# Performance work log

Hardware: AMD Instinct MI355X
Metric: run time of the kernel (lower is better)

The kernel has to match this reference:

```python
import jax, jax.numpy as jnp
import numpy as np

B, S, D, NH = 4, 2048, 1024, 16
HD = D // NH


def setup_inputs() -> dict:
    key = jax.random.key(0)
    ks = jax.random.split(key, 8)
    inp = {
        'value': jax.random.normal(ks[0], (B, S, D), jnp.float32),
        'key_t': jax.random.normal(ks[1], (B, S, D), jnp.float32),
        'query': jax.random.normal(ks[2], (B, S, D), jnp.float32),
        'mask': jnp.ones((B, 1, 1, S), jnp.int32),
        # nn.Linear weights (stored as [out, in]; y = x @ W.T). bias=False for q/k/v.
        'W_q': jax.random.normal(ks[3], (D, D), jnp.float32) * (D ** -0.5),
        'W_k': jax.random.normal(ks[4], (D, D), jnp.float32) * (D ** -0.5),
        'W_v': jax.random.normal(ks[5], (D, D), jnp.float32) * (D ** -0.5),
        'W_o': jax.random.normal(ks[6], (D, D), jnp.float32) * (D ** -0.5),
        'b_o': jax.random.normal(ks[7], (D,), jnp.float32) * 0.01,
    }
    return inp


def _split_head(x):
    b, s, d = x.shape
    return x.reshape(b, s, NH, d // NH).transpose(0, 2, 1, 3)  # [B,NH,S,HD]


def reference(value, key_t, query, mask, W_q, W_k, W_v, W_o, b_o):
    # Linear projections (y = x @ W.T), then split heads
    q = _split_head(query @ W_q.T)  # [B,NH,S,HD]
    k = _split_head(key_t @ W_k.T)
    v = _split_head(value @ W_v.T)

    q = q * (HD ** -0.5)
    att = jnp.einsum('bhqd,bhkd->bhqk', q, k)  # [B,NH,S,S]
    att = jnp.where(mask == 0, -jnp.inf, att)
    att = jax.nn.softmax(att, axis=-1)
    # dropout_ratio = 0.0 -> identity (eval mode)
    ctx = jnp.einsum('bhqk,bhkd->bhqd', att, v)  # [B,NH,S,HD]

    ctx = ctx.transpose(0, 2, 1, 3).reshape(B, S, D)  # concat heads
    out = ctx @ W_o.T + b_o
    out = jax.nn.gelu(out, approximate=False)  # nn.GELU default = exact erf
    return out
```

## Files before the change

### kernel.cpp

```cpp
#include <hip/hip_runtime.h>
#include <hip/hip_bf16.h>

typedef __bf16 bf16;
typedef __bf16 bf16x8 __attribute__((ext_vector_type(8)));
typedef __bf16 bf16x4 __attribute__((ext_vector_type(4)));
typedef float f32x4 __attribute__((ext_vector_type(4)));
typedef float f32x16 __attribute__((ext_vector_type(16)));
typedef unsigned int uint;

#define NB 4
#define NS 2048
#define ND 1024
#define NHH 16
#define NHD 64

__device__ __forceinline__ void gload_lds16(const void* g, void* l) {
  __builtin_amdgcn_global_load_lds((const __attribute__((address_space(1))) void*)g,
                                   (__attribute__((address_space(3))) void*)l, 16, 0, 0);
}

__device__ __forceinline__ f32x4 mfma16(bf16x8 a, bf16x8 b, f32x4 c) {
  return __builtin_amdgcn_mfma_f32_16x16x32_bf16(a, b, c, 0, 0, 0);
}
__device__ __forceinline__ f32x16 mfma32(bf16x8 a, bf16x8 b, f32x16 c) {
  return __builtin_amdgcn_mfma_f32_32x32x16_bf16(a, b, c, 0, 0, 0);
}
__device__ __forceinline__ uint cvtpk(float lo, float hi) {
  uint r;
  asm("v_cvt_pk_bf16_f32 %0, %1, %2" : "=v"(r) : "v"(lo), "v"(hi));
  return r;
}
__device__ __forceinline__ void swap32u(uint& a, uint& b) {
  asm("v_permlane32_swap_b32 %0, %1" : "+v"(a), "+v"(b));
}
__device__ __forceinline__ float expv(float x) {
  float r;
  asm("v_exp_f32 %0, %1" : "=v"(r) : "v"(x));
  return r;
}
#define BARRIER()                          \
  do {                                     \
    asm volatile("" ::: "memory");         \
    __builtin_amdgcn_s_barrier();          \
    asm volatile("" ::: "memory");         \
  } while (0)

__global__ __launch_bounds__(256) void cvt_bf16(const float4* __restrict__ in,
                                                bf16x4* __restrict__ out,
                                                float scale, int n4) {
  int i = blockIdx.x * 256 + threadIdx.x;
  if (i < n4) {
    float4 v = in[i];
    bf16x4 o;
    o[0] = (bf16)(v.x * scale);
    o[1] = (bf16)(v.y * scale);
    o[2] = (bf16)(v.z * scale);
    o[3] = (bf16)(v.w * scale);
    out[i] = o;
  }
}

__global__ __launch_bounds__(256) void prep(
    const float4* __restrict__ w0, const float4* __restrict__ w1,
    const float4* __restrict__ w2, const float4* __restrict__ w3,
    bf16x4* __restrict__ wout, float scale0, int n4each,
    const int* __restrict__ m, float* __restrict__ mb,
    uint* __restrict__ cleanw, int nmask) {
  const int bid = blockIdx.x;
  if (bid < 4096) {
    int i = bid * 256 + threadIdx.x;
    int w = i / n4each;
    int j = i - w * n4each;
    const float4* src = (w == 0) ? w0 : (w == 1) ? w1 : (w == 2) ? w2 : w3;
    float sc = (w == 0) ? scale0 : 1.0f;
    float4 v = src[j];
    bf16x4 o;
    o[0] = (bf16)(v.x * sc);
    o[1] = (bf16)(v.y * sc);
    o[2] = (bf16)(v.z * sc);
    o[3] = (bf16)(v.w * sc);
    wout[i] = o;
  } else if (bid < 4128) {
    int i = (bid - 4096) * 256 + threadIdx.x;
    if (i < nmask) mb[i] = m[i] ? 0.0f : -3e38f;
  } else {
    int i = threadIdx.x;
    if (i < 128) {
      const int* p = m + i * 64;
      int all1 = 1;
#pragma unroll
      for (int j = 0; j < 64; j += 4) {
        int4 v = *(const int4*)(p + j);
        all1 &= (v.x && v.y && v.z && v.w) ? 1 : 0;
      }
      unsigned long long bal = __ballot(all1);
      int wv = i >> 6, lane = i & 63;
      if (lane == 0) {
        cleanw[2 * wv] = (uint)bal;
        cleanw[2 * wv + 1] = (uint)(bal >> 32);
      }
    }
  }
}

template <int EPI>
__global__ __launch_bounds__(256) void gemm8(
    const bf16* __restrict__ A, const bf16* __restrict__ Bw,
    bf16* __restrict__ Cb, float* __restrict__ Cf,
    const float* __restrict__ bias, int M, int N, int K) {
  __shared__ bf16 As[3][4096];
  __shared__ bf16 Bs[3][4096];
  bf16* As0 = &As[0][0];
  bf16* Bs0 = &Bs[0][0];
  const int tid = threadIdx.x;
  const int lane = tid & 63, wv = tid >> 6;
  const int wr = wv >> 1, wc = wv & 1;
  const int g = lane >> 4, r = lane & 15;
  const int nx = N >> 7;
  const int chunk = gridDim.x >> 3;
  const int bid = blockIdx.x;
  const int wg = (bid & 7) * chunk + (bid >> 3);
  const int colBase = (wg % nx) * 128;
  const int rowBase = (wg / nx) * 128;

  const int sRow = wv * 16 + (lane >> 2);
  const int sK = ((lane & 3) ^ ((lane >> 3) & 3)) * 8;
  const bf16* aj0 = A + (long)(rowBase + sRow) * K + sK;
  const bf16* aj1 = aj0 + 64L * K;
  const bf16* bj0 = Bw + (long)(colBase + sRow) * K + sK;
  const bf16* bj1 = bj0 + 64L * K;

#define GSTAGE(bi, kk)                                      \
  do {                                                      \
    gload_lds16(aj0 + (kk), As0 + (bi) * 4096 + wv * 512);  \
    gload_lds16(aj1 + (kk), As0 + (bi) * 4096 + 2048 + wv * 512); \
    gload_lds16(bj0 + (kk), Bs0 + (bi) * 4096 + wv * 512);  \
    gload_lds16(bj1 + (kk), Bs0 + (bi) * 4096 + 2048 + wv * 512); \
  } while (0)

  f32x4 acc[4][4] = {};
  const int gs = (g ^ ((r >> 1) & 3)) * 8;

  GSTAGE(0, 0);
  GSTAGE(1, 32);
  int cur = 0, nxt2 = 2;

  for (int k0 = 0; k0 < K; k0 += 32) {
    if (k0 + 32 < K) {
      asm volatile("s_waitcnt vmcnt(4)" ::: "memory");
    } else {
      asm volatile("s_waitcnt vmcnt(0)" ::: "memory");
    }
    BARRIER();
    __builtin_amdgcn_sched_barrier(0);
    if (k0 + 64 < K) GSTAGE(nxt2, k0 + 64);

    const bf16* Ac = As0 + cur * 4096;
    const bf16* Bc = Bs0 + cur * 4096;
    bf16x8 af[4], bfr[4];
#pragma unroll
    for (int m = 0; m < 4; m++)
      af[m] = *(const bf16x8*)(Ac + (wr * 64 + m * 16 + r) * 32 + gs);
#pragma unroll
    for (int n = 0; n < 4; n++)
      bfr[n] = *(const bf16x8*)(Bc + (wc * 64 + n * 16 + r) * 32 + gs);
    __builtin_amdgcn_s_setprio(1);
#pragma unroll
    for (int m = 0; m < 4; m++)
#pragma unroll
      for (int n = 0; n < 4; n++)
        acc[m][n] = mfma16(af[m], bfr[n], acc[m][n]);
    __builtin_amdgcn_s_setprio(0);
    cur = (cur == 2) ? 0 : cur + 1;
    nxt2 = (nxt2 == 2) ? 0 : nxt2 + 1;
  }
#undef GSTAGE

  if (EPI == 0) {
#pragma unroll
    for (int m = 0; m < 4; m++)
#pragma unroll
      for (int n = 0; n < 4; n++)
#pragma unroll
        for (int q = 0; q < 4; q++) {
          int row = rowBase + wr * 64 + m * 16 + 4 * g + q;
          int col = colBase + wc * 64 + n * 16 + r;
          Cb[(long)row * N + col] = (bf16)acc[m][n][q];
        }
  } else if (EPI == 1) {
    const int b = rowBase >> 11;
    const int sbase = (rowBase & 2047) + wr * 64;
#pragma unroll
    for (int m = 0; m < 4; m++) {
#pragma unroll
      for (int n = 0; n < 4; n++) {
        int col = colBase + wc * 64 + n * 16 + r;
        int h = col >> 6, d = col & 63;
        bf16x4 pk;
#pragma unroll
        for (int q = 0; q < 4; q++) pk[q] = (bf16)acc[m][n][q];
        *(bf16x4*)(Cb + ((long)(b * NHH + h) * NHD + d) * NS + sbase + m * 16 + 4 * g) = pk;
      }
    }
  } else {
#pragma unroll
    for (int m = 0; m < 4; m++)
#pragma unroll
      for (int n = 0; n < 4; n++)
#pragma unroll
        for (int q = 0; q < 4; q++) {
          int row = rowBase + wr * 64 + m * 16 + 4 * g + q;
          int col = colBase + wc * 64 + n * 16 + r;
          float v = acc[m][n][q] + bias[col];
          v = 0.5f * v * (1.0f + erff(v * 0.70710678118654752f));
          Cf[(long)row * N + col] = v;
        }
  }
}

__global__ __launch_bounds__(512) void attn_fwd4(
    const bf16* __restrict__ Q, const bf16* __restrict__ K,
    const bf16* __restrict__ Vt, const float* __restrict__ mbias,
    const uint* __restrict__ cleanw, bf16* __restrict__ ctx) {
  __shared__ bf16 Ks[3][64 * 64];
  __shared__ bf16 Vs[3][64 * 64];
  bf16* Ks0 = &Ks[0][0];
  bf16* Vs0 = &Vs[0][0];
  const int tid = threadIdx.x;
  const int lane = tid & 63, wv = tid >> 6;
  const int ql = lane & 31, hi = lane >> 5;
  const int g = blockIdx.x;
  const int gx = (g & 63) >> 3;
  const int bh = ((g >> 6) << 3) | (g & 7);
  const int b = bh >> 4, h = bh & 15;
  const int q0 = gx * 256 + wv * 32;

  const bf16* Qp = Q + ((long)(b * NS + q0 + ql)) * ND + h * NHD;
  const bf16* Kp = K + ((long)b * NS) * ND + h * NHD;
  const bf16* Vp = Vt + (long)bh * NHD * NS;
  const float* mbp = mbias + b * NS;
  const uint cw = cleanw[b];

  bf16x8 qf[4];
#pragma unroll
  for (int cd = 0; cd < 4; cd++)
    qf[cd] = *(const bf16x8*)(Qp + cd * 16 + hi * 8);

  bf16x8 ones;
#pragma unroll
  for (int i = 0; i < 8; i++) ones[i] = (bf16)1.0f;

  f32x16 o[2] = {};
  f32x16 ldn = {};

  const int Lrow = wv * 8 + (lane >> 3);
  const int scb = ((lane & 7) * 16) ^ ((Lrow & 7) << 4);
  const bf16* kS = Kp + (long)Lrow * ND + (scb >> 1);
  const bf16* vS = Vp + (long)Lrow * NS + (scb >> 1);

#define ASTAGE(bi, sv)                                        \
  do {                                                        \
    gload_lds16(kS + (long)(sv) * ND, Ks0 + (bi) * 4096 + wv * 512); \
    gload_lds16(vS + (sv), Vs0 + (bi) * 4096 + wv * 512);     \
  } while (0)

  const int swz = (ql & 7) << 4;

  ASTAGE(0, 0);
  int cur = 0, nxt = 1;

  for (int s0 = 0; s0 < NS; s0 += 64) {
    if (s0 + 64 < NS) {
      ASTAGE(nxt, s0 + 64);
      asm volatile("s_waitcnt vmcnt(2)" ::: "memory");
    } else {
      asm volatile("s_waitcnt vmcnt(0)" ::: "memory");
    }
    BARRIER();
    __builtin_amdgcn_sched_barrier(0);
    const char* KsB = (const char*)(Ks0 + cur * 4096);
    const char* VsB = (const char*)(Vs0 + cur * 4096);

    f32x16 st0 = {}, st1 = {};
    __builtin_amdgcn_s_setprio(1);
#pragma unroll
    for (int cd = 0; cd < 4; cd++) {
      bf16x8 kf0 = *(const bf16x8*)(KsB + ql * 128 + ((cd * 32 + hi * 16) ^ swz));
      st0 = mfma32(kf0, qf[cd], st0);
      bf16x8 kf1 = *(const bf16x8*)(KsB + (32 + ql) * 128 + ((cd * 32 + hi * 16) ^ swz));
      st1 = mfma32(kf1, qf[cd], st1);
    }
    __builtin_amdgcn_s_setprio(0);

    if (!((cw >> (s0 >> 6)) & 1)) {
#pragma unroll
      for (int t = 0; t < 4; t++) {
        float4 m0 = *(const float4*)(mbp + s0 + t * 8 + hi * 4);
        st0[4 * t + 0] += m0.x;
        st0[4 * t + 1] += m0.y;
        st0[4 * t + 2] += m0.z;
        st0[4 * t + 3] += m0.w;
        float4 m1 = *(const float4*)(mbp + s0 + 32 + t * 8 + hi * 4);
        st1[4 * t + 0] += m1.x;
        st1[4 * t + 1] += m1.y;
        st1[4 * t + 2] += m1.z;
        st1[4 * t + 3] += m1.w;
      }
    }

#pragma unroll
    for (int i = 0; i < 16; i++) {
      st0[i] = expv(st0[i]);
      st1[i] = expv(st1[i]);
    }

    union {
      uint u[16];
      bf16x8 f[4];
    } pw;
    {
      uint c0 = cvtpk(st0[0], st0[1]), c1 = cvtpk(st0[4], st0[5]);
      swap32u(c0, c1);
      uint d0 = cvtpk(st0[2], st0[3]), d1 = cvtpk(st0[6], st0[7]);
      swap32u(d0, d1);
      pw.u[0] = c0; pw.u[1] = d0; pw.u[2] = c1; pw.u[3] = d1;
      uint e0 = cvtpk(st0[8], st0[9]), e1 = cvtpk(st0[12], st0[13]);
      swap32u(e0, e1);
      uint f0 = cvtpk(st0[10], st0[11]), f1 = cvtpk(st0[14], st0[15]);
      swap32u(f0, f1);
      pw.u[4] = e0; pw.u[5] = f0; pw.u[6] = e1; pw.u[7] = f1;
    }
    {
      uint c0 = cvtpk(st1[0], st1[1]), c1 = cvtpk(st1[4], st1[5]);
      swap32u(c0, c1);
      uint d0 = cvtpk(st1[2], st1[3]), d1 = cvtpk(st1[6], st1[7]);
      swap32u(d0, d1);
      pw.u[8] = c0; pw.u[9] = d0; pw.u[10] = c1; pw.u[11] = d1;
      uint e0 = cvtpk(st1[8], st1[9]), e1 = cvtpk(st1[12], st1[13]);
      swap32u(e0, e1);
      uint f0 = cvtpk(st1[10], st1[11]), f1 = cvtpk(st1[14], st1[15]);
      swap32u(f0, f1);
      pw.u[12] = e0; pw.u[13] = f0; pw.u[14] = e1; pw.u[15] = f1;
    }

    __builtin_amdgcn_s_setprio(1);
#pragma unroll
    for (int dt = 0; dt < 2; dt++) {
#pragma unroll
      for (int ck = 0; ck < 4; ck++) {
        bf16x8 vf = *(const bf16x8*)(VsB + (dt * 32 + ql) * 128 +
                                     ((ck * 32 + hi * 16) ^ swz));
        o[dt] = mfma32(vf, pw.f[ck], o[dt]);
      }
    }
#pragma unroll
    for (int ck = 0; ck < 4; ck++) ldn = mfma32(ones, pw.f[ck], ldn);
    __builtin_amdgcn_s_setprio(0);
    cur = nxt;
    nxt = (nxt == 2) ? 0 : nxt + 1;
  }
#undef ASTAGE

  const float invL = 1.0f / ldn[0];
  bf16* op = ctx + ((long)(b * NS + q0 + ql)) * ND + h * NHD;
#pragma unroll
  for (int dt = 0; dt < 2; dt++) {
#pragma unroll
    for (int t = 0; t < 4; t++) {
      bf16x4 pk;
#pragma unroll
      for (int i = 0; i < 4; i++) pk[i] = (bf16)(o[dt][t * 4 + i] * invL);
      *(bf16x4*)(op + dt * 32 + t * 8 + hi * 4) = pk;
    }
  }
}

extern "C" void kernel_launch(void* const* d_in, const int* in_sizes, int n_in,
                              void* d_out, int out_size, void* d_ws, size_t ws_size,
                              hipStream_t stream) {
  const float* value = (const float*)d_in[0];
  const float* key_t = (const float*)d_in[1];
  const float* query = (const float*)d_in[2];
  const int* mask = (const int*)d_in[3];
  const float* W_q = (const float*)d_in[4];
  const float* W_k = (const float*)d_in[5];
  const float* W_v = (const float*)d_in[6];
  const float* W_o = (const float*)d_in[7];
  const float* b_o = (const float*)d_in[8];
  float* out = (float*)d_out;

  char* ws = (char*)d_ws;
  bf16* Axb = (bf16*)(ws + 0);
  bf16* ctx = (bf16*)(ws + 0);
  bf16* wb = (bf16*)(ws + (16UL << 20));
  bf16* Qb = (bf16*)(ws + (24UL << 20));
  bf16* Kb = (bf16*)(ws + (40UL << 20));
  bf16* Vtb = (bf16*)(ws + (56UL << 20));
  float* mbias = (float*)(ws + (72UL << 20));
  uint* cleanwd = (uint*)(ws + (72UL << 20) + 32768);

  const int nX4 = (NB * NS * ND) / 4;
  const int nW4 = (ND * ND) / 4;
  const float hscale = 0.125f * 1.44269504088896f;

  prep<<<4129, 256, 0, stream>>>((const float4*)W_q, (const float4*)W_k,
                                 (const float4*)W_v, (const float4*)W_o,
                                 (bf16x4*)wb, hscale, nW4,
                                 mask, mbias, cleanwd, NB * NS);
  bf16* wqb = wb;
  bf16* wkb = wb + 1L * ND * ND;
  bf16* wvb = wb + 2L * ND * ND;
  bf16* wob = wb + 3L * ND * ND;

  const int ggrid = ((NB * NS) / 128) * (ND / 128);

  cvt_bf16<<<nX4 / 256, 256, 0, stream>>>((const float4*)query, (bf16x4*)Axb, 1.0f, nX4);
  gemm8<0><<<ggrid, 256, 0, stream>>>(Axb, wqb, Qb, nullptr, nullptr, NB * NS, ND, ND);

  cvt_bf16<<<nX4 / 256, 256, 0, stream>>>((const float4*)key_t, (bf16x4*)Axb, 1.0f, nX4);
  gemm8<0><<<ggrid, 256, 0, stream>>>(Axb, wkb, Kb, nullptr, nullptr, NB * NS, ND, ND);

  cvt_bf16<<<nX4 / 256, 256, 0, stream>>>((const float4*)value, (bf16x4*)Axb, 1.0f, nX4);
  gemm8<1><<<ggrid, 256, 0, stream>>>(Axb, wvb, Vtb, nullptr, nullptr, NB * NS, ND, ND);

  attn_fwd4<<<512, 512, 0, stream>>>(Qb, Kb, Vtb, mbias, cleanwd, ctx);

  gemm8<2><<<ggrid, 256, 0, stream>>>(ctx, wob, nullptr, out, b_o, NB * NS, ND, ND);
}
```

Measured before the change: 223.3 us.

## Fuse fp32->bf16 input conversion into a single batched QKV projection GEMM

```diff
diff --git a/kernel.cpp b/kernel.cpp
--- a/kernel.cpp
+++ b/kernel.cpp
@@ -44,21 +44,6 @@
     __builtin_amdgcn_s_barrier();          \
     asm volatile("" ::: "memory");         \
   } while (0)
-
-__global__ __launch_bounds__(256) void cvt_bf16(const float4* __restrict__ in,
-                                                bf16x4* __restrict__ out,
-                                                float scale, int n4) {
-  int i = blockIdx.x * 256 + threadIdx.x;
-  if (i < n4) {
-    float4 v = in[i];
-    bf16x4 o;
-    o[0] = (bf16)(v.x * scale);
-    o[1] = (bf16)(v.y * scale);
-    o[2] = (bf16)(v.z * scale);
-    o[3] = (bf16)(v.w * scale);
-    out[i] = o;
-  }
-}
 
 __global__ __launch_bounds__(256) void prep(
     const float4* __restrict__ w0, const float4* __restrict__ w1,
@@ -103,6 +88,142 @@
   }
 }
 
+__global__ __launch_bounds__(256) void gemm_qkv(
+    const float* __restrict__ Aq, const float* __restrict__ Ak,
+    const float* __restrict__ Av, const bf16* __restrict__ Wb,
+    bf16* __restrict__ Qb, bf16* __restrict__ Kb, bf16* __restrict__ Vtb) {
+  __shared__ bf16 Bs[3][4096];
+  bf16* Bs0 = &Bs[0][0];
+  const int tid = threadIdx.x;
+  const int lane = tid & 63, wv = tid >> 6;
+  const int wr = wv >> 1, wc = wv & 1;
+  const int g = lane >> 4, r = lane & 15;
+  const int bid = blockIdx.x;
+  const int wg = (bid & 7) * 192 + (bid >> 3);
+  const int z = wg >> 9;
+  const int t5 = wg & 511;
+  const int colBase = (t5 & 7) * 128;
+  const int rowBase = (t5 >> 3) * 128;
+
+  const float* A = (z == 0) ? Aq : (z == 1) ? Ak : Av;
+  const bf16* Bw = Wb + (long)z * ND * ND;
+
+  const float* a0p = A + (long)(rowBase + wr * 64 + 0 * 16 + r) * ND + 8 * g;
+  const float* a1p = A + (long)(rowBase + wr * 64 + 1 * 16 + r) * ND + 8 * g;
+  const float* a2p = A + (long)(rowBase + wr * 64 + 2 * 16 + r) * ND + 8 * g;
+  const float* a3p = A + (long)(rowBase + wr * 64 + 3 * 16 + r) * ND + 8 * g;
+
+  const int sRow = wv * 16 + (lane >> 2);
+  const int sK = ((lane & 3) ^ ((lane >> 3) & 3)) * 8;
+  const bf16* bj0 = Bw + (long)(colBase + sRow) * ND + sK;
+  const bf16* bj1 = bj0 + 64L * ND;
+
+#define ALOAD(S, kk)                       \
+  do {                                     \
+    S[0] = *(const float4*)(a0p + (kk));   \
+    S[1] = *(const float4*)(a0p + (kk) + 4); \
+    S[2] = *(const float4*)(a1p + (kk));   \
+    S[3] = *(const float4*)(a1p + (kk) + 4); \
+    S[4] = *(const float4*)(a2p + (kk));   \
+    S[5] = *(const float4*)(a2p + (kk) + 4); \
+    S[6] = *(const float4*)(a3p + (kk));   \
+    S[7] = *(const float4*)(a3p + (kk) + 4); \
+  } while (0)
+#define BSTAGE(bi, kk)                                           \
+  do {                                                           \
+    gload_lds16(bj0 + (kk), Bs0 + (bi) * 4096 + wv * 512);       \
+    gload_lds16(bj1 + (kk), Bs0 + (bi) * 4096 + 2048 + wv * 512); \
+  } while (0)
+#define ACVT(S)                                                  \
+  do {                                                           \
+    _Pragma("unroll") for (int m = 0; m < 4; m++) {              \
+      af[m][0] = (bf16)S[2 * m].x;                               \
+      af[m][1] = (bf16)S[2 * m].y;                               \
+      af[m][2] = (bf16)S[2 * m].z;                               \
+      af[m][3] = (bf16)S[2 * m].w;                               \
+      af[m][4] = (bf16)S[2 * m + 1].x;                           \
+      af[m][5] = (bf16)S[2 * m + 1].y;                           \
+      af[m][6] = (bf16)S[2 * m + 1].z;                           \
+      af[m][7] = (bf16)S[2 * m + 1].w;                           \
+    }                                                            \
+  } while (0)
+#define QKV_STEP(S)                                              \
+  do {                                                           \
+    if (t == 31)                                                 \
+      asm volatile("s_waitcnt vmcnt(0)" ::: "memory");           \
+    else                                                         \
+      asm volatile("s_waitcnt vmcnt(10)" ::: "memory");          \
+    BARRIER();                                                   \
+    __builtin_amdgcn_sched_barrier(0);                           \
+    bf16x8 af[4];                                                \
+    ACVT(S);  \
+    if (t + 2 < 32) {                                            \
+      ALOAD(S, (t + 2) * 32);                                    \
+      BSTAGE(nxt2, (t + 2) * 32);                                \
+    }                                                            \
+    __builtin_amdgcn_sched_barrier(0);                           \
+    const bf16* Bc = Bs0 + cur * 4096;                           \
+    __builtin_amdgcn_s_setprio(1);                               \
+    _Pragma("unroll") for (int n = 0; n < 4; n++) {              \
+      bf16x8 bfr = *(const bf16x8*)(Bc + (wc * 64 + n * 16 + r) * 32 + gs); \
+      _Pragma("unroll") for (int m = 0; m < 4; m++)              \
+          acc[m][n] = mfma16(af[m], bfr, acc[m][n]);             \
+    }                                                            \
+    __builtin_amdgcn_s_setprio(0);                               \
+    cur = (cur == 2) ? 0 : cur + 1;                              \
+    nxt2 = (nxt2 == 2) ? 0 : nxt2 + 1;                           \
+    t++;                                                         \
+  } while (0)
+
+  f32x4 acc[4][4] = {};
+  const int gs = (g ^ ((r >> 1) & 3)) * 8;
+  float4 aE[8], aO[8];
+
+  ALOAD(aE, 0);
+  BSTAGE(0, 0);
+  ALOAD(aO, 32);
+  BSTAGE(1, 32);
+  int cur = 0, nxt2 = 2, t = 0;
+
+  for (int i = 0; i < 16; i++) {
+    QKV_STEP(aE);
+    QKV_STEP(aO);
+  }
+#undef QKV_STEP
+#undef ACVT
+#undef BSTAGE
+#undef ALOAD
+
+  if (z <= 1) {
+    bf16* C = z ? Kb : Qb;
+#pragma unroll
+    for (int m = 0; m < 4; m++)
+#pragma unroll
+      for (int n = 0; n < 4; n++)
+#pragma unroll
+        for (int q = 0; q < 4; q++) {
+          int row = rowBase + wr * 64 + m * 16 + 4 * g + q;
+          int col = colBase + wc * 64 + n * 16 + r;
+          C[(long)row * ND + col] = (bf16)acc[m][n][q];
+        }
+  } else {
+    const int b = rowBase >> 11;
+    const int sbase = (rowBase & 2047) + wr * 64;
+#pragma unroll
+    for (int m = 0; m < 4; m++) {
+#pragma unroll
+      for (int n = 0; n < 4; n++) {
+        int col = colBase + wc * 64 + n * 16 + r;
+        int h = col >> 6, d = col & 63;
+        bf16x4 pk;
+#pragma unroll
+        for (int q = 0; q < 4; q++) pk[q] = (bf16)acc[m][n][q];
+        *(bf16x4*)(Vtb + ((long)(b * NHH + h) * NHD + d) * NS + sbase + m * 16 + 4 * g) = pk;
+      }
+    }
+  }
+}
+
 template <int EPI>
 __global__ __launch_bounds__(256) void gemm8(
     const bf16* __restrict__ A, const bf16* __restrict__ Bw,
@@ -187,21 +308,6 @@
           int col = colBase + wc * 64 + n * 16 + r;
           Cb[(long)row * N + col] = (bf16)acc[m][n][q];
         }
-  } else if (EPI == 1) {
-    const int b = rowBase >> 11;
-    const int sbase = (rowBase & 2047) + wr * 64;
-#pragma unroll
-    for (int m = 0; m < 4; m++) {
-#pragma unroll
-      for (int n = 0; n < 4; n++) {
-        int col = colBase + wc * 64 + n * 16 + r;
-        int h = col >> 6, d = col & 63;
-        bf16x4 pk;
-#pragma unroll
-        for (int q = 0; q < 4; q++) pk[q] = (bf16)acc[m][n][q];
-        *(bf16x4*)(Cb + ((long)(b * NHH + h) * NHD + d) * NS + sbase + m * 16 + 4 * g) = pk;
-      }
-    }
   } else {
 #pragma unroll
     for (int m = 0; m < 4; m++)
@@ -390,7 +496,6 @@
   float* out = (float*)d_out;
 
   char* ws = (char*)d_ws;
-  bf16* Axb = (bf16*)(ws + 0);
   bf16* ctx = (bf16*)(ws + 0);
   bf16* wb = (bf16*)(ws + (16UL << 20));
   bf16* Qb = (bf16*)(ws + (24UL << 20));
@@ -399,7 +504,6 @@
   float* mbias = (float*)(ws + (72UL << 20));
   uint* cleanwd = (uint*)(ws + (72UL << 20) + 32768);
 
-  const int nX4 = (NB * NS * ND) / 4;
   const int nW4 = (ND * ND) / 4;
   const float hscale = 0.125f * 1.44269504088896f;
 
@@ -407,23 +511,12 @@
                                  (const float4*)W_v, (const float4*)W_o,
                                  (bf16x4*)wb, hscale, nW4,
                                  mask, mbias, cleanwd, NB * NS);
-  bf16* wqb = wb;
-  bf16* wkb = wb + 1L * ND * ND;
-  bf16* wvb = wb + 2L * ND * ND;
   bf16* wob = wb + 3L * ND * ND;
 
-  const int ggrid = ((NB * NS) / 128) * (ND / 128);
-
-  cvt_bf16<<<nX4 / 256, 256, 0, stream>>>((const float4*)query, (bf16x4*)Axb, 1.0f, nX4);
-  gemm8<0><<<ggrid, 256, 0, stream>>>(Axb, wqb, Qb, nullptr, nullptr, NB * NS, ND, ND);
-
-  cvt_bf16<<<nX4 / 256, 256, 0, stream>>>((const float4*)key_t, (bf16x4*)Axb, 1.0f, nX4);
-  gemm8<0><<<ggrid, 256, 0, stream>>>(Axb, wkb, Kb, nullptr, nullptr, NB * NS, ND, ND);
-
-  cvt_bf16<<<nX4 / 256, 256, 0, stream>>>((const float4*)value, (bf16x4*)Axb, 1.0f, nX4);
-  gemm8<1><<<ggrid, 256, 0, stream>>>(Axb, wvb, Vtb, nullptr, nullptr, NB * NS, ND, ND);
+  gemm_qkv<<<1536, 256, 0, stream>>>(query, key_t, value, wb, Qb, Kb, Vtb);
 
   attn_fwd4<<<512, 512, 0, stream>>>(Qb, Kb, Vtb, mbias, cleanwd, ctx);
 
-  gemm8<2><<<ggrid, 256, 0, stream>>>(ctx, wob, nullptr, out, b_o, NB * NS, ND, ND);
-}
+  gemm8<2><<<((NB * NS) / 128) * (ND / 128), 256, 0, stream>>>(
+      ctx, wob, nullptr, out, b_o, NB * NS, ND, ND);
+}
```

New measurement: 427.7 us. +91.6%, slower.
